# Performance work log

Hardware: AMD Instinct MI355X
Metric: run time of the kernel (lower is better)

The kernel has to match this reference:

```python
import jax, jax.numpy as jnp
import numpy as np

V = 50257      # num_class
H = 512        # hid_size
EMB = 256      # embedding_size
E = 128        # emb_cond_size
COND_RANGE = (10, 20, 30)
NCSEQ = 100    # num_cond_seq_class
T, B = 64, 32
TC = 32        # cond_seq length


def _gru_scan(x, h0, Wih, Whh, bih, bhh):
    """PyTorch-convention GRU. x: [T,B,in], h0: [B,Hd]. Gate order: r,z,n."""
    Hd = h0.shape[-1]
    xw = jnp.einsum('tbi,gi->tbg', x, Wih) + bih  # [T,B,3H]

    def step(h, xw_t):
        hw = h @ Whh.T + bhh
        r = jax.nn.sigmoid(xw_t[:, :Hd] + hw[:, :Hd])
        z = jax.nn.sigmoid(xw_t[:, Hd:2 * Hd] + hw[:, Hd:2 * Hd])
        n = jnp.tanh(xw_t[:, 2 * Hd:] + r * hw[:, 2 * Hd:])
        hn = (1.0 - z) * n + z * h
        return hn, hn

    hT, outs = jax.lax.scan(step, h0, xw)
    return outs, hT


def setup_inputs() -> dict:
    key = jax.random.key(0)
    ks = jax.random.split(key, 24)
    s = 0.02
    inp = {
        'input_data': jax.random.randint(ks[0], (T, B), 0, V),
        'condition': jnp.stack([jax.random.randint(ks[1 + i], (B,), 0, COND_RANGE[i]) for i in range(3)], 0),
        'cond_seq': jax.random.randint(ks[4], (TC, B), 0, NCSEQ),
        'emb_cond_0': jax.random.normal(ks[5], (COND_RANGE[0], E)) * s,
        'emb_cond_1': jax.random.normal(ks[6], (COND_RANGE[1], E)) * s,
        'emb_cond_2': jax.random.normal(ks[7], (COND_RANGE[2], E)) * s,
        'cond_seq_emb': jax.random.normal(ks[8], (NCSEQ, E)) * s,
        'embedding': jax.random.normal(ks[9], (V, EMB)) * s,
        'attn_W': jax.random.normal(ks[10], (H, E + H)) * s,
        'attn_b': jnp.zeros((H,), jnp.float32),
        'v_W': jax.random.normal(ks[11], (1, H)) * s,
        'gru_Wih': jax.random.normal(ks[12], (3 * H, EMB)) * s,
        'gru_Whh': jax.random.normal(ks[13], (3 * H, H)) * s,
        'gru_bih': jnp.zeros((3 * H,), jnp.float32),
        'gru_bhh': jnp.zeros((3 * H,), jnp.float32),
        'cgru_Wih': jax.random.normal(ks[14], (3 * E, E)) * s,
        'cgru_Whh': jax.random.normal(ks[15], (3 * E, E)) * s,
        'cgru_bih': jnp.zeros((3 * E,), jnp.float32),
        'cgru_bhh': jnp.zeros((3 * E,), jnp.float32),
        'dense_W': jax.random.normal(ks[16], (V, E + EMB + H)) * s,
        'dense_b': jnp.zeros((V,), jnp.float32),
    }
    return inp


def reference(input_data, condition, cond_seq,
              emb_cond_0, emb_cond_1, emb_cond_2, cond_seq_emb, embedding,
              attn_W, attn_b, v_W,
              gru_Wih, gru_Whh, gru_bih, gru_bhh,
              cgru_Wih, cgru_Whh, cgru_bih, cgru_bhh,
              dense_W, dense_b):
    Tl, Bl = input_data.shape
    # conditional embeddings: [num_cond, B, E]
    tables = (emb_cond_0, emb_cond_1, emb_cond_2)
    cond_emb = jnp.stack([tables[i][condition[i]] for i in range(3)], axis=0)
    # conditional sequence GRU encoder: [TC, B, E]
    cseq_in = cond_seq_emb[cond_seq]
    cseq_out, _ = _gru_scan(cseq_in, jnp.zeros((Bl, E), cseq_in.dtype),
                            cgru_Wih, cgru_Whh, cgru_bih, cgru_bhh)
    enc = jnp.concatenate([cond_emb, cseq_out], axis=0)  # [S, B, E]
    enc_b = jnp.transpose(enc, (1, 0, 2))                # [B, S, E]

    # Bahdanau attention: split attn weight into encoder/decoder parts
    W_e = attn_W[:, :E]   # [H, E]
    W_h = attn_W[:, E:]   # [H, H]
    enc_proj = jnp.einsum('bse,he->bsh', enc_b, W_e)     # precompute once

    x_emb = embedding[input_data]                        # [T, B, EMB]
    xw = jnp.einsum('tbi,gi->tbg', x_emb, gru_Wih) + gru_bih  # [T, B, 3H]

    def step(h, inputs):
        xe_t, xw_t = inputs
        # attention against previous hidden h
        score = jnp.tanh(enc_proj + (h @ W_h.T + attn_b)[:, None, :]) @ v_W[0]  # [B,S]
        w = jax.nn.softmax(score, axis=1)
        c = jnp.einsum('bs,bse->be', w, enc_b)           # [B, E]
        # GRU cell
        hw = h @ gru_Whh.T + gru_bhh
        r = jax.nn.sigmoid(xw_t[:, :H] + hw[:, :H])
        z = jax.nn.sigmoid(xw_t[:, H:2 * H] + hw[:, H:2 * H])
        n = jnp.tanh(xw_t[:, 2 * H:] + r * hw[:, 2 * H:])
        hn = (1.0 - z) * n + z * h
        # output head uses context, input embedding and PREVIOUS hidden h
        logits = jnp.concatenate([c, xe_t, h], axis=-1) @ dense_W.T + dense_b
        pred = jax.nn.log_softmax(logits, axis=-1)
        return hn, (pred, w)

    h0 = jnp.zeros((Bl, H), x_emb.dtype)
    hT, (total_pred, weights) = jax.lax.scan(step, h0, (x_emb, xw))
    return total_pred, hT[None, :, :], weights


if __name__ == '__main__':
    out = reference(**setup_inputs())
    print([o.shape for o in out])
```

## Files before the change

kernel.cpp:

```cpp
#include <hip/hip_runtime.h>
#include <hip/hip_bf16.h>
#include <hip/hip_cooperative_groups.h>
#include <math.h>

namespace cg = cooperative_groups;

#define Tt 64
#define Bb 32
#define Hh 512
#define EMBe 256
#define Ee 128
#define Ss 35
#define Vv 50257
#define Kk 896
#define TCc 32
#define VPAD 50304

typedef __bf16 bf16_t;
typedef __bf16 bf16x4 __attribute__((ext_vector_type(4)));
typedef __bf16 bf16x8 __attribute__((ext_vector_type(8)));
typedef float f32x4 __attribute__((ext_vector_type(4)));

#define POIS32 0x7FC07FC0u

__device__ __forceinline__ float sigf(float x){ return 1.f/(1.f + expf(-x)); }

__device__ __forceinline__ void gll16(const void* g, void* l){
  __builtin_amdgcn_global_load_lds(
      (const __attribute__((address_space(1))) unsigned int*)g,
      (__attribute__((address_space(3))) unsigned int*)l, 16, 0, 0);
}

#define DOT4(acc, W_, H_) acc += (W_).x*(H_).x + (W_).y*(H_).y + (W_).z*(H_).z + (W_).w*(H_).w

__global__ void k_cond_emb(const int* __restrict__ cond, const float* __restrict__ t0,
                           const float* __restrict__ t1, const float* __restrict__ t2,
                           float* __restrict__ enc){
  int g = blockIdx.x*blockDim.x + threadIdx.x;
  if (g >= 3*Bb*Ee) return;
  int i = g/(Bb*Ee); int b = (g/Ee)%Bb; int e = g%Ee;
  const float* tbl = (i==0)? t0 : (i==1)? t1 : t2;
  int ci = cond[i*Bb + b];
  enc[(size_t)i*Bb*Ee + b*Ee + e] = tbl[(size_t)ci*Ee + e];
}

__global__ void k_cxw(const int* __restrict__ cond_seq, const float* __restrict__ cemb,
                      const float* __restrict__ Wih, const float* __restrict__ bih,
                      float* __restrict__ cxw){
  __shared__ float es[Ee];
  int row = blockIdx.x; int tid = threadIdx.x;
  int idx = cond_seq[row];
  es[tid] = cemb[(size_t)idx*Ee + tid];
  __syncthreads();
  const float4* hp = (const float4*)es;
  for (int q = 0; q < 3; ++q){
    int g = q*Ee + tid;
    const float4* wr = (const float4*)(Wih + (size_t)g*Ee);
    float acc = bih[g];
    #pragma unroll 8
    for (int k = 0; k < Ee/4; ++k){ float4 w4 = wr[k]; float4 h4 = hp[k]; DOT4(acc, w4, h4); }
    cxw[(size_t)row*(3*Ee) + g] = acc;
  }
}

__global__ void k_xemb(const int* __restrict__ input_data, const float* __restrict__ emb,
                       bf16_t* __restrict__ xe){
  int row = blockIdx.x, tid = threadIdx.x;
  int idx = input_data[row];
  xe[(size_t)row*EMBe + tid] = (bf16_t)emb[(size_t)idx*EMBe + tid];
}

__global__ void k_ctrans(const float* __restrict__ W, float* __restrict__ WT){
  int idx = blockIdx.x*256 + threadIdx.x;
  if (idx >= 3*Ee*Ee) return;
  int g = idx/Ee, k = idx%Ee;
  WT[(size_t)k*(3*Ee) + g] = W[idx];
}

__global__ void k_cseq_scan(const float* __restrict__ cxw, const float* __restrict__ WT,
                            const float* __restrict__ bhh, float* __restrict__ enc){
  __shared__ float hs[Ee];
  int b = blockIdx.x; int j = threadIdx.x;
  hs[j] = 0.f; __syncthreads();
  float b0 = bhh[j], b1 = bhh[Ee+j], b2 = bhh[2*Ee+j];
  for (int t = 0; t < TCc; ++t){
    const float* xp = cxw + ((size_t)t*Bb + b)*(3*Ee);
    float a0=b0, a1=b1, a2=b2;
    #pragma unroll 4
    for (int k = 0; k < Ee; ++k){
      float hk = hs[k];
      const float* wr = WT + (size_t)k*(3*Ee);
      a0 += hk * wr[j];
      a1 += hk * wr[Ee + j];
      a2 += hk * wr[2*Ee + j];
    }
    float r = sigf(xp[j] + a0);
    float z = sigf(xp[Ee + j] + a1);
    float n = tanhf(xp[2*Ee + j] + r*a2);
    float hcur = hs[j];
    float hn = (1.f - z)*n + z*hcur;
    __syncthreads();
    hs[j] = hn;
    enc[(size_t)(3+t)*Bb*Ee + b*Ee + j] = hn;
    __syncthreads();
  }
}

__global__ void k_encproj(const float* __restrict__ enc, const float* __restrict__ attn_W,
                          float* __restrict__ enc_proj){
  __shared__ float es[Ee];
  int blk = blockIdx.x; int tid = threadIdx.x;
  int b = blk/Ss, s = blk%Ss;
  if (tid < Ee) es[tid] = enc[(size_t)s*Bb*Ee + b*Ee + tid];
  __syncthreads();
  const float4* hp = (const float4*)es;
  for (int q = 0; q < 2; ++q){
    int hh = q*256 + tid;
    const float4* wr = (const float4*)(attn_W + (size_t)hh*(Ee+Hh));
    float acc = 0.f;
    #pragma unroll 8
    for (int k = 0; k < Ee/4; ++k){ float4 w4 = wr[k]; float4 h4 = hp[k]; DOT4(acc, w4, h4); }
    enc_proj[(size_t)blk*Hh + hh] = acc;
  }
}

#define HSLOT (Bb*Hh)

__global__ void k_poison(bf16_t* __restrict__ hsteps){
  size_t i = (size_t)blockIdx.x*256 + threadIdx.x;
  size_t total = (size_t)(Tt+1)*HSLOT/2;
  if (i >= total) return;
  unsigned v = (i < HSLOT/2) ? 0u : POIS32;
  __hip_atomic_store((unsigned*)hsteps + i, v, __ATOMIC_RELAXED, __HIP_MEMORY_SCOPE_AGENT);
}

#define SCAN_BLOCKS_L 128
#define SCAN_WORK 16
#define SCAN_THREADS 384
#define WSL_STRIDE 520
#define HST_STRIDE 520
#define GW_STRIDE 104
#define SCAN_LDS (96*WSL_STRIDE*2 + Bb*HST_STRIDE*2 + Bb*GW_STRIDE*4)
#define NCH 11

__global__ __launch_bounds__(SCAN_THREADS) void k_scan_coop(
    const float* __restrict__ xw, const float* __restrict__ Whh,
    const float* __restrict__ bhh, float* __restrict__ h_all,
    bf16_t* __restrict__ hsteps, const float* __restrict__ Wd,
    bf16_t* __restrict__ Wb, int wbf){
  extern __shared__ char smem[];
  const int tid = threadIdx.x;
  const int blk = blockIdx.x;

  if (blk >= SCAN_WORK){
    if (wbf){
      size_t total = (size_t)VPAD*Kk/8;
      size_t stride = (size_t)(SCAN_BLOCKS_L - SCAN_WORK)*SCAN_THREADS;
      for (size_t c = (size_t)(blk - SCAN_WORK)*SCAN_THREADS + tid; c < total; c += stride){
        size_t i = c*8;
        size_t row = i / Kk;
        int col = (int)(i % Kk);
        bf16x8 o;
        if (row < Vv){
          float4 f0 = *(const float4*)(Wd + i);
          float4 f1 = *(const float4*)(Wd + i + 4);
          o[0]=(bf16_t)f0.x; o[1]=(bf16_t)f0.y; o[2]=(bf16_t)f0.z; o[3]=(bf16_t)f0.w;
          o[4]=(bf16_t)f1.x; o[5]=(bf16_t)f1.y; o[6]=(bf16_t)f1.z; o[7]=(bf16_t)f1.w;
        } else {
          #pragma unroll
          for (int k = 0; k < 8; ++k) o[k] = (bf16_t)0.f;
        }
        int kk = col >> 6, u = (col & 63) >> 3;
        int rs = (int)(row & 7);
        *(bf16x8*)(Wb + row*Kk + (kk << 6) + ((u ^ rs) << 3)) = o;
      }
    }
    return;
  }

  bf16_t* Wsl = (bf16_t*)smem;
  bf16_t* hst = (bf16_t*)(smem + 96*WSL_STRIDE*2);
  float*  gw  = (float*) (smem + 96*WSL_STRIDE*2 + Bb*HST_STRIDE*2);
  const int c0 = blk*32;

  for (int lr = 0; lr < 96; ++lr){
    int g = lr >> 5, i = lr & 31;
    const float* src = Whh + ((size_t)g*Hh + c0 + i)*Hh;
    for (int c = tid; c < Hh; c += SCAN_THREADS)
      Wsl[lr*WSL_STRIDE + c] = (bf16_t)src[c];
  }
  for (int idx = tid; idx < Bb*16; idx += SCAN_THREADS){
    int b = idx >> 4, u = idx & 15;
    float* hp = &h_all[(size_t)b*Hh + c0 + u*2];
    hp[0] = 0.f; hp[1] = 0.f;
  }

  const int npair = (tid < 128) ? 2 : 1;
  int pb[2], pc[2];
  float bh0[2][2], bh1[2][2], bh2[2][2], hreg[2][2];
  for (int p = 0; p < npair; ++p){
    int pid = tid + p*SCAN_THREADS;
    pb[p] = pid >> 4; pc[p] = (pid & 15)*2;
    for (int c = 0; c < 2; ++c){
      int j = c0 + pc[p] + c;
      bh0[p][c] = bhh[j]; bh1[p][c] = bhh[Hh + j]; bh2[p][c] = bhh[2*Hh + j];
      hreg[p][c] = 0.f;
    }
  }
  __syncthreads();

  const int wid = tid >> 6, lane = tid & 63;
  const int l15 = lane & 15, l4 = lane >> 4;

  for (int t = 0; t < Tt; ++t){
    {
      const unsigned long long* hinU = (const unsigned long long*)(hsteps + (size_t)t*HSLOT);
      unsigned long long v[NCH];
      int nmine = 0;
      #pragma unroll
      for (int k = 0; k < NCH; ++k){
        int idx = tid + k*SCAN_THREADS;
        if (idx < Bb*Hh/4){
          v[k] = __hip_atomic_load(hinU + idx, __ATOMIC_RELAXED, __HIP_MEMORY_SCOPE_AGENT);
          nmine = k + 1;
        }
      }
      #pragma unroll
      for (int k = 0; k < NCH; ++k){
        if (k < nmine){
          int idx = tid + k*SCAN_THREADS;
          while ((unsigned)v[k] == POIS32 || (unsigned)(v[k] >> 32) == POIS32){
            __builtin_amdgcn_s_sleep(1);
            v[k] = __hip_atomic_load(hinU + idx, __ATOMIC_RELAXED, __HIP_MEMORY_SCOPE_AGENT);
          }
        }
      }
      #pragma unroll
      for (int k = 0; k < NCH; ++k){
        if (k < nmine){
          int idx = tid + k*SCAN_THREADS;
          int b = idx >> 7, c4 = idx & 127;
          *((unsigned long long*)(hst + (size_t)b*HST_STRIDE) + c4) = v[k];
        }
      }
    }
    __syncthreads();

    f32x4 acc0 = {0.f,0.f,0.f,0.f}, acc1 = {0.f,0.f,0.f,0.f};
    #pragma unroll
    for (int ks = 0; ks < 16; ++ks){
      bf16x8 bfr = *(const bf16x8*)(Wsl + (wid*16 + l15)*WSL_STRIDE + ks*32 + l4*8);
      bf16x8 a0  = *(const bf16x8*)(hst + l15*HST_STRIDE        + ks*32 + l4*8);
      bf16x8 a1  = *(const bf16x8*)(hst + (16 + l15)*HST_STRIDE + ks*32 + l4*8);
      acc0 = __builtin_amdgcn_mfma_f32_16x16x32_bf16(a0, bfr, acc0, 0, 0, 0);
      acc1 = __builtin_amdgcn_mfma_f32_16x16x32_bf16(a1, bfr, acc1, 0, 0, 0);
    }
    #pragma unroll
    for (int i = 0; i < 4; ++i){
      gw[(l4*4 + i)*GW_STRIDE + wid*16 + l15]        = acc0[i];
      gw[(16 + l4*4 + i)*GW_STRIDE + wid*16 + l15]   = acc1[i];
    }
    __syncthreads();

    unsigned* houtU = (unsigned*)(hsteps + (size_t)(t+1)*HSLOT);
    for (int p = 0; p < npair; ++p){
      int b = pb[p], cl = pc[p];
      const float* xp = xw + ((size_t)t*Bb + b)*(3*Hh);
      float hn2[2];
      #pragma unroll
      for (int c = 0; c < 2; ++c){
        int j = c0 + cl + c;
        float gr = gw[b*GW_STRIDE + cl + c]      + bh0[p][c];
        float gz = gw[b*GW_STRIDE + 32 + cl + c] + bh1[p][c];
        float gn = gw[b*GW_STRIDE + 64 + cl + c] + bh2[p][c];
        float r = sigf(xp[j] + gr);
        float z = sigf(xp[Hh + j] + gz);
        float n = tanhf(xp[2*Hh + j] + r*gn);
        float hn = (1.f - z)*n + z*hreg[p][c];
        hreg[p][c] = hn; hn2[c] = hn;
      }
      unsigned u0 = (unsigned)__builtin_bit_cast(unsigned short, (bf16_t)hn2[0]);
      unsigned u1 = (unsigned)__builtin_bit_cast(unsigned short, (bf16_t)hn2[1]);
      __hip_atomic_store(houtU + ((b*Hh + c0 + cl) >> 1), u0 | (u1 << 16),
                         __ATOMIC_RELAXED, __HIP_MEMORY_SCOPE_AGENT);
    }
    for (int p = 0; p < npair; ++p){
      int b = pb[p], cl = pc[p];
      float* hp = &h_all[((size_t)(t+1)*Bb + b)*Hh + c0 + cl];
      hp[0] = hreg[p][0]; hp[1] = hreg[p][1];
    }
  }
}

#define SG_LDS (256*64*2)
#define SWZ(rowv, uv) (((size_t)(rowv))*64 + ((((uv) ^ ((rowv)&7)))<<3))

template<int KTOT, int LDB>
__global__ __launch_bounds__(256) void k_sgemm(const bf16_t* __restrict__ A,
                                               const float* __restrict__ B,
                                               const float* __restrict__ bias,
                                               float* __restrict__ C, int N){
  extern __shared__ char smem[];
  bf16_t* As = (bf16_t*)smem;
  bf16_t* Ws = As + 128*64;
  const int tid = threadIdx.x, bid = blockIdx.x;
  const int mt = bid & 15, nt = bid >> 4;
  const int m0 = mt*128, n0 = nt*128;
  const int srow = tid >> 1, sub = (tid & 1)*4;
  const int NKK2 = KTOT/64;

  int4 aR[4]; float4 wF[8];
#define SLOADA(KK) { \
    const int4* p = (const int4*)(A + (size_t)(m0 + srow)*KTOT + (KK)*64 + sub*8); \
    aR[0]=p[0]; aR[1]=p[1]; aR[2]=p[2]; aR[3]=p[3]; }
#define SLOADW(KK) { \
    const float4* p = (const float4*)(B + (size_t)(n0 + srow)*LDB + (KK)*64 + sub*8); \
    _Pragma("unroll") for (int r = 0; r < 8; ++r) wF[r] = p[r]; }
#define SSTORES() { \
    _Pragma("unroll") \
    for (int j = 0; j < 4; ++j) \
      *(int4*)(As + SWZ(srow, sub + j)) = aR[j]; \
    _Pragma("unroll") for (int j = 0; j < 4; ++j){ \
      bf16x8 p8; \
      p8[0]=(bf16_t)wF[2*j].x; p8[1]=(bf16_t)wF[2*j].y; p8[2]=(bf16_t)wF[2*j].z; p8[3]=(bf16_t)wF[2*j].w; \
      p8[4]=(bf16_t)wF[2*j+1].x; p8[5]=(bf16_t)wF[2*j+1].y; p8[6]=(bf16_t)wF[2*j+1].z; p8[7]=(bf16_t)wF[2*j+1].w; \
      *(bf16x8*)(Ws + SWZ(srow, sub + j)) = p8; \
    } }

  const int wave = tid >> 6, lane = tid & 63;
  const int l15 = lane & 15, l4 = lane >> 4;
  const int mh = (wave >> 1)*64, nh = (wave & 1)*64;

  f32x4 acc[4][4];
  #pragma unroll
  for (int i = 0; i < 4; ++i)
    #pragma unroll
    for (int j = 0; j < 4; ++j) acc[i][j] = (f32x4){0.f,0.f,0.f,0.f};

  SLOADA(0); SLOADW(0);
  SSTORES();
  __syncthreads();
  for (int kk = 0; kk < NKK2; ++kk){
    if (kk + 1 < NKK2){ SLOADA(kk + 1); SLOADW(kk + 1); }
    #pragma unroll
    for (int k32 = 0; k32 < 2; ++k32){
      const int u = k32*4 + l4;
      bf16x8 aF[4], bF[4];
      #pragma unroll
      for (int mf = 0; mf < 4; ++mf)
        aF[mf] = *(const bf16x8*)(As + SWZ(mh + mf*16 + l15, u));
      #pragma unroll
      for (int nf = 0; nf < 4; ++nf)
        bF[nf] = *(const bf16x8*)(Ws + SWZ(nh + nf*16 + l15, u));
      #pragma unroll
      for (int mf = 0; mf < 4; ++mf)
        #pragma unroll
        for (int nf = 0; nf < 4; ++nf)
          acc[mf][nf] = __builtin_amdgcn_mfma_f32_16x16x32_bf16(aF[mf], bF[nf], acc[mf][nf], 0, 0, 0);
    }
    __syncthreads();
    if (kk + 1 < NKK2){
      SSTORES();
      __syncthreads();
    }
  }
  #pragma unroll
  for (int mf = 0; mf < 4; ++mf){
    #pragma unroll
    for (int nf = 0; nf < 4; ++nf){
      int v = n0 + nh + nf*16 + l15;
      float bv = bias[v];
      int m = m0 + mh + mf*16 + l4*4;
      #pragma unroll
      for (int i = 0; i < 4; ++i)
        C[(size_t)(m + i)*N + v] = acc[mf][nf][i] + bv;
    }
  }
#undef SLOADA
#undef SLOADW
#undef SSTORES
}

__global__ void k_score(const float* __restrict__ hw_attn, const float* __restrict__ enc_proj,
                        const float* __restrict__ enc, const float* __restrict__ vW,
                        float* __restrict__ w_out, float* __restrict__ c_all){
  __shared__ float hws[Hh];
  __shared__ float sc[Ss];
  __shared__ float wsm[Ss];
  int row = blockIdx.x, lane = threadIdx.x;
  int b = row & (Bb-1);
  for (int k = lane; k < Hh; k += 64) hws[k] = hw_attn[(size_t)row*Hh + k];
  __syncthreads();
  for (int s = 0; s < Ss; ++s){
    const float* ep = enc_proj + ((size_t)b*Ss + s)*Hh;
    float acc = 0.f;
    for (int k = lane; k < Hh; k += 64) acc += tanhf(ep[k] + hws[k]) * vW[k];
    #pragma unroll
    for (int off = 32; off > 0; off >>= 1) acc += __shfl_xor(acc, off);
    if (lane == 0) sc[s] = acc;
  }
  __syncthreads();
  float val = (lane < Ss) ? sc[lane] : -3.0e38f;
  float mx = val;
  #pragma unroll
  for (int off = 32; off > 0; off >>= 1) mx = fmaxf(mx, __shfl_xor(mx, off));
  float e = (lane < Ss) ? expf(val - mx) : 0.f;
  float sm = e;
  #pragma unroll
  for (int off = 32; off > 0; off >>= 1) sm += __shfl_xor(sm, off);
  float w = e / sm;
  if (lane < Ss){ w_out[(size_t)row*Ss + lane] = w; wsm[lane] = w; }
  __syncthreads();
  for (int q = 0; q < 2; ++q){
    int ee = q*64 + lane;
    float acc = 0.f;
    #pragma unroll
    for (int s = 0; s < Ss; ++s) acc += wsm[s]*enc[(size_t)s*Bb*Ee + b*Ee + ee];
    c_all[(size_t)row*Ee + ee] = acc;
  }
}

__global__ void k_abuild(const int* __restrict__ input_data, const float* __restrict__ c_all,
                         const float* __restrict__ embedding, const float* __restrict__ h_all,
                         bf16_t* __restrict__ A){
  int row = blockIdx.x, tid = threadIdx.x;
  int xidx = input_data[row];
  bf16_t* Ar = A + (size_t)row*Kk;
  int rs = row & 7;
  for (int col = tid; col < Kk; col += 256){
    float v;
    if (col < Ee) v = c_all[(size_t)row*Ee + col];
    else if (col < Ee + EMBe) v = embedding[(size_t)xidx*EMBe + (col - Ee)];
    else v = h_all[(size_t)row*Hh + (col - Ee - EMBe)];
    int kk = col >> 6, u = (col & 63) >> 3, e = col & 7;
    Ar[(kk << 6) + ((u ^ rs) << 3) + e] = (bf16_t)v;
  }
}

#define BM 128
#define BN 128
#define BK 64
#define NKK (Kk/BK)
#define BUFSZ ((BM + BN)*BK)
#define GEMM_LDS (2*BUFSZ*2)

template<int WBF>
__global__ __launch_bounds__(256) void k_gemm7(const bf16_t* __restrict__ A,
                                               const void* __restrict__ Wsrc,
                                               const float* __restrict__ bias,
                                               float* __restrict__ out){
  extern __shared__ char smem[];
  const int tid = threadIdx.x;
  const int bid = blockIdx.x;
  const int mt = bid & 15, nt = bid >> 4;
  const int m0 = mt*BM, n0 = nt*BN;
  const int wave = tid >> 6, lane = tid & 63;
  const int l15 = lane & 15, l4 = lane >> 4;
  const int mh = (wave >> 1)*64, nh = (wave & 1)*64;

  f32x4 acc[4][4];
  #pragma unroll
  for (int i = 0; i < 4; ++i)
    #pragma unroll
    for (int j = 0; j < 4; ++j) acc[i][j] = (f32x4){0.f,0.f,0.f,0.f};

  if (WBF){
    const char* Ag = (const char*)A;
    const char* Wg = (const char*)Wsrc;
    bf16_t* bufs = (bf16_t*)smem;
    const int grow = tid >> 3;
    const size_t gcol = (size_t)(tid & 7)*16;
    {
      char* Asb = (char*)bufs;
      char* Wsb = Asb + BM*BK*2;
      #pragma unroll
      for (int j = 0; j < 4; ++j){
        gll16(Ag + (size_t)(m0 + j*32 + grow)*(Kk*2) + gcol, Asb + j*4096 + tid*16);
        gll16(Wg + (size_t)(n0 + j*32 + grow)*(Kk*2) + gcol, Wsb + j*4096 + tid*16);
      }
    }
    int cur = 0;
    for (int kk = 0; kk < NKK; ++kk){
      __syncthreads();
      if (kk + 1 < NKK){
        size_t ko = (size_t)(kk + 1)*128;
        char* Asb = (char*)(bufs + (cur ^ 1)*BUFSZ);
        char* Wsb = Asb + BM*BK*2;
        #pragma unroll
        for (int j = 0; j < 4; ++j){
          gll16(Ag + (size_t)(m0 + j*32 + grow)*(Kk*2) + ko + gcol, Asb + j*4096 + tid*16);
          gll16(Wg + (size_t)(n0 + j*32 + grow)*(Kk*2) + ko + gcol, Wsb + j*4096 + tid*16);
        }
      }
      const bf16_t* As = bufs + cur*BUFSZ;
      const bf16_t* Ws = As + BM*BK;
      #pragma unroll
      for (int k32 = 0; k32 < 2; ++k32){
        const int u = k32*4 + l4;
        bf16x8 aF[4], bF[4];
        #pragma unroll
        for (int mf = 0; mf < 4; ++mf)
          aF[mf] = *(const bf16x8*)(As + SWZ(mh + mf*16 + l15, u));
        #pragma unroll
        for (int nf = 0; nf < 4; ++nf)
          bF[nf] = *(const bf16x8*)(Ws + SWZ(nh + nf*16 + l15, u));
        #pragma unroll
        for (int mf = 0; mf < 4; ++mf)
          #pragma unroll
          for (int nf = 0; nf < 4; ++nf)
            acc[mf][nf] = __builtin_amdgcn_mfma_f32_16x16x32_bf16(aF[mf], bF[nf], acc[mf][nf], 0, 0, 0);
      }
      cur ^= 1;
    }
  } else {
    bf16_t* As = (bf16_t*)smem;
    bf16_t* Ws = As + BM*BK;
    const int srow = tid >> 1, sub = (tid & 1)*4;
    int4 aR[4]; float4 wF[8];
    const float* Wf = (const float*)Wsrc;
#define LOADA(KK) { \
    const int4* p = (const int4*)(A + (size_t)(m0 + srow)*Kk + (KK)*BK + sub*8); \
    aR[0]=p[0]; aR[1]=p[1]; aR[2]=p[2]; aR[3]=p[3]; }
#define LOADW(KK) { \
    int vrow = n0 + srow; \
    if (vrow < Vv){ \
      const float4* p = (const float4*)(Wf + (size_t)vrow*Kk + (KK)*BK + sub*8); \
      _Pragma("unroll") for (int r = 0; r < 8; ++r) wF[r] = p[r]; \
    } else { \
      _Pragma("unroll") for (int r = 0; r < 8; ++r) wF[r] = make_float4(0.f,0.f,0.f,0.f); \
    } }
#define STORES() { \
    _Pragma("unroll") \
    for (int j = 0; j < 4; ++j) \
      *(int4*)(As + (size_t)srow*64 + (size_t)(sub + j)*8) = aR[j]; \
    _Pragma("unroll") for (int j = 0; j < 4; ++j){ \
      bf16x8 p8; \
      p8[0]=(bf16_t)wF[2*j].x; p8[1]=(bf16_t)wF[2*j].y; p8[2]=(bf16_t)wF[2*j].z; p8[3]=(bf16_t)wF[2*j].w; \
      p8[4]=(bf16_t)wF[2*j+1].x; p8[5]=(bf16_t)wF[2*j+1].y; p8[6]=(bf16_t)wF[2*j+1].z; p8[7]=(bf16_t)wF[2*j+1].w; \
      *(bf16x8*)(Ws + SWZ(srow, sub + j)) = p8; \
    } }
    LOADA(0); LOADW(0);
    STORES();
    __syncthreads();
    for (int kk = 0; kk < NKK; ++kk){
      if (kk + 1 < NKK){ LOADA(kk + 1); LOADW(kk + 1); }
      #pragma unroll
      for (int k32 = 0; k32 < 2; ++k32){
        const int u = k32*4 + l4;
        bf16x8 aF[4], bF[4];
        #pragma unroll
        for (int mf = 0; mf < 4; ++mf)
          aF[mf] = *(const bf16x8*)(As + SWZ(mh + mf*16 + l15, u));
        #pragma unroll
        for (int nf = 0; nf < 4; ++nf)
          bF[nf] = *(const bf16x8*)(Ws + SWZ(nh + nf*16 + l15, u));
        #pragma unroll
        for (int mf = 0; mf < 4; ++mf)
          #pragma unroll
          for (int nf = 0; nf < 4; ++nf)
            acc[mf][nf] = __builtin_amdgcn_mfma_f32_16x16x32_bf16(aF[mf], bF[nf], acc[mf][nf], 0, 0, 0);
      }
      __syncthreads();
      if (kk + 1 < NKK){
        STORES();
        __syncthreads();
      }
    }
#undef LOADA
#undef LOADW
#undef STORES
  }
  #pragma unroll
  for (int mf = 0; mf < 4; ++mf){
    #pragma unroll
    for (int nf = 0; nf < 4; ++nf){
      int v = n0 + nh + nf*16 + l15;
      if (v < Vv){
        float bv = bias[v];
        int m = m0 + mh + mf*16 + l4*4;
        #pragma unroll
        for (int i = 0; i < 4; ++i){
          out[(size_t)(m + i)*Vv + v] = acc[mf][nf][i] + bv;
        }
      }
    }
  }
}

__global__ void k_lse(const float* __restrict__ pred, float* __restrict__ lse){
  __shared__ float ms[256], ssum[256];
  int row = blockIdx.x, tid = threadIdx.x;
  const float* p = pred + (size_t)row*Vv;
  int pre = (int)(((16 - (((size_t)p) & 15)) & 15) >> 2);
  float m = -3.0e38f, s = 0.f;
  if (tid < pre){ float x = p[tid]; m = x; s = 1.f; }
  int n4 = (Vv - pre) >> 2;
  const float4* p4 = (const float4*)(p + pre);
  for (int v = tid; v < n4; v += 256){
    float4 x4 = p4[v];
    #pragma unroll
    for (int q = 0; q < 4; ++q){
      float x = (q==0)? x4.x : (q==1)? x4.y : (q==2)? x4.z : x4.w;
      if (x > m){ s = s*expf(m - x) + 1.f; m = x; }
      else s += expf(x - m);
    }
  }
  int tl = pre + n4*4 + tid;
  if (tl < Vv){ float x = p[tl]; if (x > m){ s = s*expf(m - x) + 1.f; m = x; } else s += expf(x - m); }
  ms[tid] = m; ssum[tid] = s;
  __syncthreads();
  for (int off = 128; off > 0; off >>= 1){
    if (tid < off){
      float m2 = ms[tid+off], s2 = ssum[tid+off];
      float m1 = ms[tid],     s1 = ssum[tid];
      if (m2 > m1){ s1 = s1*expf(m1 - m2) + s2; m1 = m2; }
      else s1 += s2*expf(m2 - m1);
      ms[tid] = m1; ssum[tid] = s1;
    }
    __syncthreads();
  }
  if (tid == 0) lse[row] = ms[0] + logf(ssum[0]);
}

__global__ void k_sub(float* __restrict__ pred, const float* __restrict__ lse){
  int row = blockIdx.x, tid = threadIdx.x;
  float l = lse[row];
  float* p = pred + (size_t)row*Vv;
  int pre = (int)(((16 - (((size_t)p) & 15)) & 15) >> 2);
  if (tid < pre) p[tid] -= l;
  int n4 = (Vv - pre) >> 2;
  float4* p4 = (float4*)(p + pre);
  for (int v = tid; v < n4; v += 256){
    float4 x = p4[v];
    x.x -= l; x.y -= l; x.z -= l; x.w -= l;
    p4[v] = x;
  }
  int tl = pre + n4*4 + tid;
  if (tl < Vv) p[tl] -= l;
}

__global__ void k_hT(const float* __restrict__ h_all, float* __restrict__ hT){
  int g = blockIdx.x*256 + threadIdx.x;
  if (g < Bb*Hh) hT[g] = h_all[(size_t)Tt*Bb*Hh + g];
}

extern "C" void kernel_launch(void* const* d_in, const int* in_sizes, int n_in,
                              void* d_out, int out_size, void* d_ws, size_t ws_size,
                              hipStream_t stream){
  const int*   input_data = (const int*)d_in[0];
  const int*   condition  = (const int*)d_in[1];
  const int*   cond_seq   = (const int*)d_in[2];
  const float* emb_c0     = (const float*)d_in[3];
  const float* emb_c1     = (const float*)d_in[4];
  const float* emb_c2     = (const float*)d_in[5];
  const float* cseq_emb   = (const float*)d_in[6];
  const float* embedding  = (const float*)d_in[7];
  const float* attn_W     = (const float*)d_in[8];
  const float* attn_b     = (const float*)d_in[9];
  const float* v_W        = (const float*)d_in[10];
  const float* gru_Wih    = (const float*)d_in[11];
  const float* gru_Whh    = (const float*)d_in[12];
  const float* gru_bih    = (const float*)d_in[13];
  const float* gru_bhh    = (const float*)d_in[14];
  const float* cgru_Wih   = (const float*)d_in[15];
  const float* cgru_Whh   = (const float*)d_in[16];
  const float* cgru_bih   = (const float*)d_in[17];
  const float* cgru_bhh   = (const float*)d_in[18];
  const float* dense_W    = (const float*)d_in[19];
  const float* dense_b    = (const float*)d_in[20];

  float* out    = (float*)d_out;
  float* pred   = out;
  float* hT_out = out + (size_t)Tt*Bb*Vv;
  float* w_out  = hT_out + (size_t)Bb*Hh;

  float* ws       = (float*)d_ws;
  float* h_all    = ws;
  float* xw       = h_all + (size_t)(Tt+1)*Bb*Hh;
  float* cxw      = xw + (size_t)Tt*Bb*3*Hh;
  float* enc      = cxw + (size_t)TCc*Bb*3*Ee;
  float* enc_proj = enc + (size_t)Ss*Bb*Ee;
  float* hw_attn  = enc_proj + (size_t)Bb*Ss*Hh;
  float* c_all    = hw_attn + (size_t)Tt*Bb*Hh;
  float* lse      = c_all + (size_t)Tt*Bb*Ee;
  bf16_t* Abf     = (bf16_t*)(lse + Tt*Bb);
  bf16_t* hsteps  = Abf + (size_t)Tt*Bb*Kk;
  float* WTc      = (float*)(hsteps + (size_t)(Tt+1)*HSLOT);
  int*   bar      = (int*)(WTc + 128*3*Ee);
  bf16_t* xemb    = (bf16_t*)(bar + 256);
  bf16_t* Wb      = xemb + (size_t)Tt*Bb*EMBe;
  size_t need_b   = (size_t)((char*)(Wb + (size_t)VPAD*Kk) - (char*)d_ws);
  bool use_wbf    = (ws_size >= need_b);

  k_cond_emb<<<48, 256, 0, stream>>>(condition, emb_c0, emb_c1, emb_c2, enc);
  k_cxw<<<TCc*Bb, 128, 0, stream>>>(cond_seq, cseq_emb, cgru_Wih, cgru_bih, cxw);
  k_xemb<<<Tt*Bb, 256, 0, stream>>>(input_data, embedding, xemb);
  k_sgemm<EMBe, EMBe><<<16*12, 256, SG_LDS, stream>>>(xemb, gru_Wih, gru_bih, xw, 3*Hh);
  k_ctrans<<<(3*Ee*Ee + 255)/256, 256, 0, stream>>>(cgru_Whh, WTc);
  k_cseq_scan<<<Bb, Ee, 0, stream>>>(cxw, WTc, cgru_bhh, enc);
  k_encproj<<<Bb*Ss, 256, 0, stream>>>(enc, attn_W, enc_proj);
  {
    int npb = (int)(((size_t)(Tt+1)*HSLOT/2 + 255)/256);
    k_poison<<<npb, 256, 0, stream>>>(hsteps);
  }

  (void)hipFuncSetAttribute((const void*)k_scan_coop, hipFuncAttributeMaxDynamicSharedMemorySize, SCAN_LDS);
  {
    void* xw_p = (void*)xw; void* whh_p = (void*)gru_Whh; void* bhh_p = (void*)gru_bhh;
    void* ha_p = (void*)h_all; void* hs_p = (void*)hsteps;
    void* wd_p = (void*)dense_W; void* wb_p = (void*)Wb;
    int wbf = use_wbf ? 1 : 0;
    void* args[] = {&xw_p, &whh_p, &bhh_p, &ha_p, &hs_p, &wd_p, &wb_p, &wbf};
    (void)hipLaunchCooperativeKernel((const void*)k_scan_coop, dim3(SCAN_BLOCKS_L), dim3(SCAN_THREADS),
                                     args, SCAN_LDS, stream);
  }

  k_sgemm<Hh, (Ee+Hh)><<<16*4, 256, SG_LDS, stream>>>(hsteps, attn_W + Ee, attn_b, hw_attn, Hh);
  k_score<<<Tt*Bb, 64, 0, stream>>>(hw_attn, enc_proj, enc, v_W, w_out, c_all);
  k_abuild<<<Tt*Bb, 256, 0, stream>>>(input_data, c_all, embedding, h_all, Abf);

  (void)hipFuncSetAttribute((const void*)k_gemm7<1>, hipFuncAttributeMaxDynamicSharedMemorySize, GEMM_LDS);
  (void)hipFuncSetAttribute((const void*)k_gemm7<0>, hipFuncAttributeMaxDynamicSharedMemorySize, GEMM_LDS);
  if (use_wbf){
    k_gemm7<1><<<16*((Vv + BN - 1)/BN), 256, GEMM_LDS, stream>>>(Abf, (const void*)Wb, dense_b, pred);
  } else {
    k_gemm7<0><<<16*((Vv + BN - 1)/BN), 256, GEMM_LDS, stream>>>(Abf, (const void*)dense_W, dense_b, pred);
  }

  k_lse<<<Tt*Bb, 256, 0, stream>>>(pred, lse);
  k_sub<<<Tt*Bb, 256, 0, stream>>>(pred, lse);
  k_hT<<<64, 256, 0, stream>>>(h_all, hT_out);
}
```

Baseline: 1.625 ms.

## Fuse per-tile log-sum-exp partials into GEMM epilogue, drop full-row LSE pass

The GEMM epilogue now computes per-row max and sum-exp partials for its 128-column tile, using shuffles and LDS, and writes them to a small partials buffer. A tiny combine kernel then merges the 393 partials per row into the LSE. This replaces the separate k_lse kernel that re-read the whole 2048x50257 logits matrix, saving one full read of that matrix. In exchange the GEMM epilogue gains exp work and an extra sync, and workspace layout shifts to hold the partials.

```diff
diff --git a/kernel.cpp b/kernel.cpp
--- a/kernel.cpp
+++ b/kernel.cpp
@@ -15,6 +15,7 @@
 #define Kk 896
 #define TCc 32
 #define VPAD 50304
+#define NTILE 393
 
 typedef __bf16 bf16_t;
 typedef __bf16 bf16x4 __attribute__((ext_vector_type(4)));
@@ -443,12 +444,19 @@
 #define NKK (Kk/BK)
 #define BUFSZ ((BM + BN)*BK)
 #define GEMM_LDS (2*BUFSZ*2)
+#define NEGINF (-1.0e30f)
+
+__device__ __forceinline__ void lse_comb(float& m, float& s, float om, float os){
+  if (om > m){ s = s*expf(m - om) + os; m = om; }
+  else        s = s + os*expf(om - m);
+}
 
 template<int WBF>
 __global__ __launch_bounds__(256) void k_gemm7(const bf16_t* __restrict__ A,
                                                const void* __restrict__ Wsrc,
                                                const float* __restrict__ bias,
-                                               float* __restrict__ out){
+                                               float* __restrict__ out,
+                                               float2* __restrict__ partials){
   extern __shared__ char smem[];
   const int tid = threadIdx.x;
   const int bid = blockIdx.x;
@@ -570,56 +578,71 @@
 #undef LOADW
 #undef STORES
   }
+  float bv4[4];
+  #pragma unroll
+  for (int nf = 0; nf < 4; ++nf){
+    int v = n0 + nh + nf*16 + l15;
+    bv4[nf] = (v < Vv) ? bias[v] : 0.f;
+  }
+  __syncthreads();
+  float2* epls = (float2*)smem;
   #pragma unroll
   for (int mf = 0; mf < 4; ++mf){
     #pragma unroll
-    for (int nf = 0; nf < 4; ++nf){
-      int v = n0 + nh + nf*16 + l15;
-      if (v < Vv){
-        float bv = bias[v];
-        int m = m0 + mh + mf*16 + l4*4;
-        #pragma unroll
-        for (int i = 0; i < 4; ++i){
-          out[(size_t)(m + i)*Vv + v] = acc[mf][nf][i] + bv;
+    for (int i = 0; i < 4; ++i){
+      float vals[4]; float m = NEGINF;
+      #pragma unroll
+      for (int nf = 0; nf < 4; ++nf){
+        int v = n0 + nh + nf*16 + l15;
+        float x = acc[mf][nf][i] + bv4[nf];
+        vals[nf] = (v < Vv) ? x : NEGINF;
+        if (v < Vv){
+          out[(size_t)(m0 + mh + mf*16 + l4*4 + i)*Vv + v] = x;
+          if (vals[nf] > m) m = vals[nf];
         }
       }
-    }
-  }
-}
-
-__global__ void k_lse(const float* __restrict__ pred, float* __restrict__ lse){
-  __shared__ float ms[256], ssum[256];
-  int row = blockIdx.x, tid = threadIdx.x;
-  const float* p = pred + (size_t)row*Vv;
-  int pre = (int)(((16 - (((size_t)p) & 15)) & 15) >> 2);
-  float m = -3.0e38f, s = 0.f;
-  if (tid < pre){ float x = p[tid]; m = x; s = 1.f; }
-  int n4 = (Vv - pre) >> 2;
-  const float4* p4 = (const float4*)(p + pre);
-  for (int v = tid; v < n4; v += 256){
-    float4 x4 = p4[v];
-    #pragma unroll
-    for (int q = 0; q < 4; ++q){
-      float x = (q==0)? x4.x : (q==1)? x4.y : (q==2)? x4.z : x4.w;
-      if (x > m){ s = s*expf(m - x) + 1.f; m = x; }
-      else s += expf(x - m);
-    }
-  }
-  int tl = pre + n4*4 + tid;
-  if (tl < Vv){ float x = p[tl]; if (x > m){ s = s*expf(m - x) + 1.f; m = x; } else s += expf(x - m); }
-  ms[tid] = m; ssum[tid] = s;
-  __syncthreads();
-  for (int off = 128; off > 0; off >>= 1){
-    if (tid < off){
-      float m2 = ms[tid+off], s2 = ssum[tid+off];
-      float m1 = ms[tid],     s1 = ssum[tid];
-      if (m2 > m1){ s1 = s1*expf(m1 - m2) + s2; m1 = m2; }
-      else s1 += s2*expf(m2 - m1);
-      ms[tid] = m1; ssum[tid] = s1;
-    }
-    __syncthreads();
-  }
-  if (tid == 0) lse[row] = ms[0] + logf(ssum[0]);
+      float s = 0.f;
+      #pragma unroll
+      for (int nf = 0; nf < 4; ++nf)
+        if (vals[nf] > NEGINF) s += expf(vals[nf] - m);
+      #pragma unroll
+      for (int off = 1; off < 16; off <<= 1){
+        float om = __shfl_xor(m, off);
+        float os = __shfl_xor(s, off);
+        lse_comb(m, s, om, os);
+      }
+      if (l15 == 0){
+        int rl = mh + mf*16 + l4*4 + i;
+        epls[rl*2 + (wave & 1)] = make_float2(m, s);
+      }
+    }
+  }
+  __syncthreads();
+  if (tid < BM){
+    float2 a = epls[tid*2 + 0];
+    float2 b = epls[tid*2 + 1];
+    float m = a.x, s = a.y;
+    lse_comb(m, s, b.x, b.y);
+    partials[(size_t)(m0 + tid)*512 + nt] = make_float2(m, s);
+  }
+}
+
+__global__ void k_lsecomb(const float2* __restrict__ partials, float* __restrict__ lse){
+  int row = blockIdx.x*4 + (threadIdx.x >> 6);
+  int lane = threadIdx.x & 63;
+  const float2* p = partials + (size_t)row*512;
+  float m = NEGINF, s = 0.f;
+  for (int nt = lane; nt < NTILE; nt += 64){
+    float2 v = p[nt];
+    lse_comb(m, s, v.x, v.y);
+  }
+  #pragma unroll
+  for (int off = 32; off > 0; off >>= 1){
+    float om = __shfl_xor(m, off);
+    float os = __shfl_xor(s, off);
+    lse_comb(m, s, om, os);
+  }
+  if (lane == 0) lse[row] = m + logf(s);
 }
 
 __global__ void k_sub(float* __restrict__ pred, const float* __restrict__ lse){
@@ -687,7 +710,8 @@
   bf16_t* hsteps  = Abf + (size_t)Tt*Bb*Kk;
   float* WTc      = (float*)(hsteps + (size_t)(Tt+1)*HSLOT);
   int*   bar      = (int*)(WTc + 128*3*Ee);
-  bf16_t* xemb    = (bf16_t*)(bar + 256);
+  float2* partials= (float2*)(bar + 256);
+  bf16_t* xemb    = (bf16_t*)(partials + (size_t)Tt*Bb*512);
   bf16_t* Wb      = xemb + (size_t)Tt*Bb*EMBe;
   size_t need_b   = (size_t)((char*)(Wb + (size_t)VPAD*Kk) - (char*)d_ws);
   bool use_wbf    = (ws_size >= need_b);
@@ -722,12 +746,12 @@
   (void)hipFuncSetAttribute((const void*)k_gemm7<1>, hipFuncAttributeMaxDynamicSharedMemorySize, GEMM_LDS);
   (void)hipFuncSetAttribute((const void*)k_gemm7<0>, hipFuncAttributeMaxDynamicSharedMemorySize, GEMM_LDS);
   if (use_wbf){
-    k_gemm7<1><<<16*((Vv + BN - 1)/BN), 256, GEMM_LDS, stream>>>(Abf, (const void*)Wb, dense_b, pred);
+    k_gemm7<1><<<16*((Vv + BN - 1)/BN), 256, GEMM_LDS, stream>>>(Abf, (const void*)Wb, dense_b, pred, partials);
   } else {
-    k_gemm7<0><<<16*((Vv + BN - 1)/BN), 256, GEMM_LDS, stream>>>(Abf, (const void*)dense_W, dense_b, pred);
-  }
-
-  k_lse<<<Tt*Bb, 256, 0, stream>>>(pred, lse);
+    k_gemm7<0><<<16*((Vv + BN - 1)/BN), 256, GEMM_LDS, stream>>>(Abf, (const void*)dense_W, dense_b, pred, partials);
+  }
+
+  k_lsecomb<<<Tt*Bb/4, 256, 0, stream>>>(partials, lse);
   k_sub<<<Tt*Bb, 256, 0, stream>>>(pred, lse);
   k_hT<<<64, 256, 0, stream>>>(h_all, hT_out);
 }
```

New measurement: 1.649 ms. About the same (+1.5%).
